# Kernel optimization log

Measured on AMD Instinct MI355X. Metric: run time of the kernel, lower is better.

Reference implementation:

```python
import jax, jax.numpy as jnp
import numpy as np

EPS = 1e-6

def rmsnorm(x, scale):
    return x * jax.lax.rsqrt(jnp.mean(x * x, axis=-1, keepdims=True) + EPS) * scale

def setup_inputs() -> dict:
    key = jax.random.key(0)
    ks = jax.random.split(key, 8)
    B1, B2 = 16, 64
    D, H, A = 8192, 1024, 2          # deter_size, hidden_size, action_size
    S, C, G = 32, 64, 8              # stoch_size, classes, blocks
    sc = 0.02                        # trunc-normal-ish init scale
    f32 = jnp.float32
    return dict(
        deter=jax.random.normal(ks[0], (B1, B2, D), f32),
        stoch=jax.random.normal(ks[1], (B1, B2, S, C), f32),
        action=jax.random.normal(ks[2], (B1, B2, A), f32),
        W1=(jax.random.normal(ks[3], (H, D), f32) * sc),
        b1=jnp.zeros((H,), f32),
        s1=jnp.ones((H,), f32),
        W2=(jax.random.normal(ks[4], (H, S * C), f32) * sc),
        b2=jnp.zeros((H,), f32),
        s2=jnp.ones((H,), f32),
        W3=(jax.random.normal(ks[5], (H, A), f32) * sc),
        b3=jnp.zeros((H,), f32),
        s3=jnp.ones((H,), f32),
        Wb1=(jax.random.normal(ks[6], (G, (3 * G * H + D) // G, D // G), f32) * sc),
        bb1=jnp.zeros((D,), f32),
        sb1=jnp.ones((D,), f32),
        Wb2=(jax.random.normal(ks[7], (G, D // G, 3 * D // G), f32) * sc),
        bb2=jnp.zeros((3 * D,), f32),
    )

def reference(deter, stoch, action, W1, b1, s1, W2, b2, s2, W3, b3, s3, Wb1, bb1, sb1, Wb2, bb2):
    batch_shape = deter.shape[:-1]
    D = deter.shape[-1]
    d = deter.reshape(-1, D)                       # (B, D)
    B = d.shape[0]
    G = Wb1.shape[0]
    H = W1.shape[0]
    s = stoch.reshape(B, -1)                       # (B, S*C)
    a = action.reshape(B, -1)                      # (B, A)
    a = a / jax.lax.stop_gradient(jnp.maximum(1.0, jnp.abs(a)))
    # three parallel Linear + RMSNorm + SiLU branches
    x1 = jax.nn.silu(rmsnorm(d @ W1.T + b1, s1))
    x2 = jax.nn.silu(rmsnorm(s @ W2.T + b2, s2))
    x3 = jax.nn.silu(rmsnorm(a @ W3.T + b3, s3))
    x = jnp.concatenate([x1, x2, x3], axis=-1)     # (B, 3H)
    x = jnp.broadcast_to(x[:, None, :], (B, G, 3 * H))
    x = jnp.concatenate([x, d.reshape(B, G, D // G)], axis=-1)  # (B, G, 3H + D/G)
    # block-diagonal grouped GEMM + RMSNorm + SiLU (dyn_layers=1)
    h = jnp.einsum('bgi,gio->bgo', x, Wb1).reshape(B, D) + bb1
    h = jax.nn.silu(rmsnorm(h, sb1))
    # final block-diagonal GEMM -> 3*D gate pre-activations
    y = jnp.einsum('bgi,gio->bgo', h.reshape(B, G, D // G), Wb2).reshape(B, 3 * D) + bb2
    r, c, u = jnp.split(y.reshape(B, G, -1), 3, axis=-1)        # each (B, G, D/G)
    reset = jax.nn.sigmoid(r.reshape(B, D))
    cand = jnp.tanh(reset * c.reshape(B, D))
    update = jax.nn.sigmoid(u.reshape(B, D) - 1.0)
    next_deter = update * cand + (1.0 - update) * d
    return next_deter.reshape(*batch_shape, D)
```

## Files before the change

### kernel.cpp

```cpp
#include <hip/hip_runtime.h>
#include <stdint.h>

typedef unsigned short ushort_t;
typedef __attribute__((ext_vector_type(8))) short bf16x8;
typedef __attribute__((ext_vector_type(4))) float f32x4;

#define EPS 1e-6f

__device__ __forceinline__ float b2f(ushort_t u) {
    union { uint32_t i; float f; } v; v.i = ((uint32_t)u) << 16; return v.f;
}
__device__ __forceinline__ ushort_t f2b(float f) {
    union { float f; uint32_t i; } v; v.f = f;
    uint32_t x = v.i;
    uint32_t r = (x + 0x7fffu + ((x >> 16) & 1u)) >> 16;
    return (ushort_t)r;
}

__device__ __forceinline__ void async_copy16(const void* g, void* l) {
    __builtin_amdgcn_global_load_lds(
        (const __attribute__((address_space(1))) uint32_t*)(uintptr_t)g,
        (__attribute__((address_space(3))) uint32_t*)(uintptr_t)l,
        16, 0, 0);
}

__global__ __launch_bounds__(256) void cast4_k(
    const float* __restrict__ s0, ushort_t* __restrict__ d0, int n0,
    const float* __restrict__ s1, ushort_t* __restrict__ d1, int n1,
    const float* __restrict__ s2, ushort_t* __restrict__ d2, int n2,
    const float* __restrict__ s3, ushort_t* __restrict__ d3) {
    int j = blockIdx.x * 256 + threadIdx.x;
    const float* s; ushort_t* d;
    if (j < n0) { s = s0; d = d0; }
    else if ((j -= n0) < n1) { s = s1; d = d1; }
    else if ((j -= n1) < n2) { s = s2; d = d2; }
    else { j -= n2; s = s3; d = d3; }
    float4 v = ((const float4*)s)[j];
    ushort4 o;
    o.x = f2b(v.x); o.y = f2b(v.y); o.z = f2b(v.z); o.w = f2b(v.w);
    ((ushort4*)d)[j] = o;
}

__global__ __launch_bounds__(256) void transpose_cast_k(const float* __restrict__ src,
                                                        ushort_t* __restrict__ dst,
                                                        int R, int C) {
    __shared__ float tile[32][33];
    int bat = blockIdx.z;
    int c0 = blockIdx.x * 32, r0 = blockIdx.y * 32;
    const float* s = src + (size_t)bat * R * C;
    ushort_t* d = dst + (size_t)bat * R * C;
    int tx = threadIdx.x, ty = threadIdx.y;
    float4 v = *(const float4*)&s[(size_t)(r0 + ty) * C + c0 + tx * 4];
    tile[ty][tx * 4 + 0] = v.x;
    tile[ty][tx * 4 + 1] = v.y;
    tile[ty][tx * 4 + 2] = v.z;
    tile[ty][tx * 4 + 3] = v.w;
    __syncthreads();
    ushort4 o;
    o.x = f2b(tile[tx * 4 + 0][ty]);
    o.y = f2b(tile[tx * 4 + 1][ty]);
    o.z = f2b(tile[tx * 4 + 2][ty]);
    o.w = f2b(tile[tx * 4 + 3][ty]);
    *(ushort4*)&d[(size_t)(c0 + ty) * R + r0 + tx * 4] = o;
}

template <int MODE, bool OUT_BF16, int BM, int BN, int WNW>
__global__ __launch_bounds__(WNW * 128, 2) void gemm_bt_k(
    const ushort_t* __restrict__ Aa, const ushort_t* __restrict__ Ab,
    const ushort_t* __restrict__ Bw,
    float* __restrict__ Cf, ushort_t* __restrict__ Cb,
    int lda, int ldb, int ldc, int Ksl, int k0base, int czoff) {
    constexpr int THREADS = WNW * 128;
    constexpr int MR = (BM / 2) / 16;
    constexpr int NR = (BN / WNW) / 16;
    constexpr int SR = THREADS >> 3;
    __shared__ __align__(16) ushort_t As[2][BM * 64];
    __shared__ __align__(16) ushort_t Bs[2][BN * 64];
    const int tid = threadIdx.x;

    const int gx = gridDim.x;
    const int nxy = gx * gridDim.y;
    const int flat = blockIdx.x + blockIdx.y * gx;
    const int cpx = nxy >> 3;
    const int L = (flat & 7) * cpx + (flat >> 3);
    const int bm = L % gx, bn = L / gx;
    const int bz = blockIdx.z;
    const int k0 = k0base + bz * Ksl;
    const int m0 = bm * BM, n0 = bn * BN;
    const int cz = bz * czoff;
    const int lane = tid & 63, w = tid >> 6;
    const int wm = (w & 1) * (BM / 2);
    const int wn = (w >> 1) * (BN / WNW);

    f32x4 acc[MR][NR];
#pragma unroll
    for (int i = 0; i < MR; i++)
#pragma unroll
        for (int j = 0; j < NR; j++) acc[i][j] = (f32x4){0.f, 0.f, 0.f, 0.f};

    auto a_ptr = [&](int m, int kk) -> const ushort_t* {
        if (MODE == 0) {
            return Aa + (size_t)m * lda + kk;
        } else if (MODE == 1) {
            if (kk < 3072) return Aa + (size_t)m * 3072 + kk;
            int g = n0 >> 10;
            return Ab + (size_t)m * 8192 + g * 1024 + (kk - 3072);
        } else {
            int g = n0 / 3072;
            return Aa + (size_t)m * 8192 + g * 1024 + kk;
        }
    };

    const int srow = tid >> 3;
    const int sslot = tid & 7;
    const int gco = (sslot ^ (srow & 7)) << 3;
    const int lco = sslot << 3;

    auto stage = [&](int buf, int kk) {
#pragma unroll
        for (int p = 0; p < BM / SR; ++p) {
            int r = p * SR + srow;
            async_copy16(a_ptr(m0 + r, kk + gco), &As[buf][r * 64 + lco]);
        }
#pragma unroll
        for (int p = 0; p < BN / SR; ++p) {
            int r = p * SR + srow;
            async_copy16(Bw + (size_t)(n0 + r) * ldb + kk + gco, &Bs[buf][r * 64 + lco]);
        }
    };

    const int nt = Ksl >> 6;
    stage(0, k0);
    __builtin_amdgcn_sched_barrier(0);

    const int qc = lane >> 4;
    const int rl = lane & 15;
    int cur = 0;

    for (int t = 0; t < nt; ++t) {
        if (t + 1 < nt) {
            stage(cur ^ 1, k0 + ((t + 1) << 6));
            asm volatile("s_waitcnt vmcnt(8)" ::: "memory");
        } else {
            asm volatile("s_waitcnt vmcnt(0)" ::: "memory");
        }
        __builtin_amdgcn_s_barrier();
        __builtin_amdgcn_sched_barrier(0);

#pragma unroll
        for (int h = 0; h < 2; ++h) {
            bf16x8 af[MR], bfr[NR];
#pragma unroll
            for (int i = 0; i < MR; i++) {
                int ra = wm + i * 16 + rl;
                int slot = ((h << 2) + qc) ^ (ra & 7);
                af[i] = *(const bf16x8*)&As[cur][ra * 64 + (slot << 3)];
            }
#pragma unroll
            for (int j = 0; j < NR; j++) {
                int rb = wn + j * 16 + rl;
                int slot = ((h << 2) + qc) ^ (rb & 7);
                bfr[j] = *(const bf16x8*)&Bs[cur][rb * 64 + (slot << 3)];
            }
#pragma unroll
            for (int i = 0; i < MR; i++)
#pragma unroll
                for (int j = 0; j < NR; j++)
                    acc[i][j] = __builtin_amdgcn_mfma_f32_16x16x32_bf16(af[i], bfr[j], acc[i][j], 0, 0, 0);
        }

        if (t + 1 < nt) {
            __builtin_amdgcn_sched_barrier(0);
            __builtin_amdgcn_s_barrier();
            __builtin_amdgcn_sched_barrier(0);
            cur ^= 1;
        }
    }

    const int cr = (lane >> 4) * 4, cc = lane & 15;
#pragma unroll
    for (int i = 0; i < MR; i++) {
#pragma unroll
        for (int j = 0; j < NR; j++) {
#pragma unroll
            for (int r = 0; r < 4; r++) {
                int row = m0 + wm + i * 16 + cr + r;
                int col = n0 + cz + wn + j * 16 + cc;
                float v = acc[i][j][r];
                if (OUT_BF16) {
                    Cb[(size_t)row * ldc + col] = f2b(v);
                } else {
                    Cf[(size_t)row * ldc + col] = v;
                }
            }
        }
    }
}

__global__ __launch_bounds__(256) void branch3_k(const float* __restrict__ act,
                                                 const float* __restrict__ W3,
                                                 float* __restrict__ xacc) {
    int idx = blockIdx.x * 256 + threadIdx.x;
    int b = idx >> 10, h = idx & 1023;
    float a0 = act[b * 2 + 0], a1 = act[b * 2 + 1];
    a0 = a0 / fmaxf(1.f, fabsf(a0));
    a1 = a1 / fmaxf(1.f, fabsf(a1));
    float v = a0 * W3[h * 2 + 0] + a1 * W3[h * 2 + 1];
    xacc[(size_t)b * 7168 + 6144 + h] = v;
}

__global__ __launch_bounds__(256) void norm_silu_1024_k(
    const float* __restrict__ xacc,
    const float* __restrict__ b1, const float* __restrict__ s1,
    const float* __restrict__ b2, const float* __restrict__ s2,
    const float* __restrict__ b3, const float* __restrict__ s3,
    ushort_t* __restrict__ xbf) {
    int b = blockIdx.x, c = blockIdx.y, tid = threadIdx.x;
    const float* bias = (c == 0) ? b1 : (c == 1) ? b2 : b3;
    const float* scl  = (c == 0) ? s1 : (c == 1) ? s2 : s3;
    const float* row = xacc + (size_t)b * 7168 + ((c == 0) ? 0 : (c == 1) ? 4096 : 6144);
    const int np = (c == 0) ? 4 : (c == 1) ? 2 : 1;
    float4 v = ((const float4*)row)[tid];
#pragma unroll 4
    for (int p = 1; p < np; ++p) {
        float4 t = ((const float4*)(row + p * 1024))[tid];
        v.x += t.x; v.y += t.y; v.z += t.z; v.w += t.w;
    }
    float4 bb = ((const float4*)bias)[tid];
    v.x += bb.x; v.y += bb.y; v.z += bb.z; v.w += bb.w;
    float ss = v.x * v.x + v.y * v.y + v.z * v.z + v.w * v.w;
#pragma unroll
    for (int off = 32; off > 0; off >>= 1) ss += __shfl_down(ss, off, 64);
    __shared__ float wsum[4];
    int lane = tid & 63, wid = tid >> 6;
    if (lane == 0) wsum[wid] = ss;
    __syncthreads();
    float tot = wsum[0] + wsum[1] + wsum[2] + wsum[3];
    float rms = rsqrtf(tot * (1.0f / 1024.0f) + EPS);
    float4 sc = ((const float4*)scl)[tid];
    float o0 = v.x * rms * sc.x; o0 = o0 / (1.f + __expf(-o0));
    float o1 = v.y * rms * sc.y; o1 = o1 / (1.f + __expf(-o1));
    float o2 = v.z * rms * sc.z; o2 = o2 / (1.f + __expf(-o2));
    float o3 = v.w * rms * sc.w; o3 = o3 / (1.f + __expf(-o3));
    ushort4 o; o.x = f2b(o0); o.y = f2b(o1); o.z = f2b(o2); o.w = f2b(o3);
    ((ushort4*)(xbf + (size_t)b * 3072 + c * 1024))[tid] = o;
}

__global__ __launch_bounds__(256) void norm_silu_8192_k(const float* __restrict__ hpre,
                                                        const float* __restrict__ bb1,
                                                        const float* __restrict__ sb1,
                                                        ushort_t* __restrict__ hbf) {
    int b = blockIdx.x, tid = threadIdx.x;
    const float4* src = (const float4*)(hpre + (size_t)b * 16384);
    float4 v[8];
    float ss = 0.f;
#pragma unroll
    for (int k = 0; k < 8; k++) {
        float4 t = src[tid + k * 256];
        float4 u = src[tid + k * 256 + 2048];
        t.x += u.x; t.y += u.y; t.z += u.z; t.w += u.w;
        float4 bv = ((const float4*)bb1)[tid + k * 256];
        t.x += bv.x; t.y += bv.y; t.z += bv.z; t.w += bv.w;
        v[k] = t;
        ss += t.x * t.x + t.y * t.y + t.z * t.z + t.w * t.w;
    }
#pragma unroll
    for (int off = 32; off > 0; off >>= 1) ss += __shfl_down(ss, off, 64);
    __shared__ float wsum[4];
    int lane = tid & 63, wid = tid >> 6;
    if (lane == 0) wsum[wid] = ss;
    __syncthreads();
    float tot = wsum[0] + wsum[1] + wsum[2] + wsum[3];
    float rms = rsqrtf(tot * (1.0f / 8192.0f) + EPS);
    ushort_t* dst = hbf + (size_t)b * 8192;
#pragma unroll
    for (int k = 0; k < 8; k++) {
        float4 sv = ((const float4*)sb1)[tid + k * 256];
        float o0 = v[k].x * rms * sv.x; o0 = o0 / (1.f + __expf(-o0));
        float o1 = v[k].y * rms * sv.y; o1 = o1 / (1.f + __expf(-o1));
        float o2 = v[k].z * rms * sv.z; o2 = o2 / (1.f + __expf(-o2));
        float o3 = v[k].w * rms * sv.w; o3 = o3 / (1.f + __expf(-o3));
        ushort4 o; o.x = f2b(o0); o.y = f2b(o1); o.z = f2b(o2); o.w = f2b(o3);
        ((ushort4*)dst)[tid + k * 256] = o;
    }
}

__global__ __launch_bounds__(256) void gates_k(const ushort_t* __restrict__ y,
                                               const float* __restrict__ bb2,
                                               const float* __restrict__ deter,
                                               float* __restrict__ out) {
    int idx = blockIdx.x * 256 + threadIdx.x;
    int f = idx * 4;
    int b = f >> 13, d = f & 8191;
    int g = d >> 10, j = d & 1023;
    size_t ybase = (size_t)b * 24576 + g * 3072 + j;
    ushort4 rv = *(const ushort4*)(y + ybase);
    ushort4 cv = *(const ushort4*)(y + ybase + 1024);
    ushort4 uv = *(const ushort4*)(y + ybase + 2048);
    float4 bbr = *(const float4*)(bb2 + g * 3072 + j);
    float4 bbc = *(const float4*)(bb2 + g * 3072 + 1024 + j);
    float4 bbu = *(const float4*)(bb2 + g * 3072 + 2048 + j);
    float4 dv = *(const float4*)(deter + f);
    float rr[4] = {b2f(rv.x) + bbr.x, b2f(rv.y) + bbr.y, b2f(rv.z) + bbr.z, b2f(rv.w) + bbr.w};
    float cc[4] = {b2f(cv.x) + bbc.x, b2f(cv.y) + bbc.y, b2f(cv.z) + bbc.z, b2f(cv.w) + bbc.w};
    float uu[4] = {b2f(uv.x) + bbu.x, b2f(uv.y) + bbu.y, b2f(uv.z) + bbu.z, b2f(uv.w) + bbu.w};
    float dd[4] = {dv.x, dv.y, dv.z, dv.w};
    float oo[4];
#pragma unroll
    for (int t = 0; t < 4; t++) {
        float reset = 1.f / (1.f + __expf(-rr[t]));
        float cand = tanhf(reset * cc[t]);
        float upd = 1.f / (1.f + __expf(-(uu[t] - 1.f)));
        oo[t] = upd * cand + (1.f - upd) * dd[t];
    }
    float4 o; o.x = oo[0]; o.y = oo[1]; o.z = oo[2]; o.w = oo[3];
    *(float4*)(out + f) = o;
}

extern "C" void kernel_launch(void* const* d_in, const int* in_sizes, int n_in,
                              void* d_out, int out_size, void* d_ws, size_t ws_size,
                              hipStream_t stream) {
    const float* deter = (const float*)d_in[0];
    const float* stoch = (const float*)d_in[1];
    const float* action = (const float*)d_in[2];
    const float* W1 = (const float*)d_in[3];
    const float* b1 = (const float*)d_in[4];
    const float* s1 = (const float*)d_in[5];
    const float* W2 = (const float*)d_in[6];
    const float* b2 = (const float*)d_in[7];
    const float* s2 = (const float*)d_in[8];
    const float* W3 = (const float*)d_in[9];
    const float* b3 = (const float*)d_in[10];
    const float* s3 = (const float*)d_in[11];
    const float* Wb1 = (const float*)d_in[12];
    const float* bb1 = (const float*)d_in[13];
    const float* sb1 = (const float*)d_in[14];
    const float* Wb2 = (const float*)d_in[15];
    const float* bb2 = (const float*)d_in[16];
    float* out = (float*)d_out;

    char* ws = (char*)d_ws;
    ushort_t* dbf   = (ushort_t*)(ws + 0);
    ushort_t* sbf   = (ushort_t*)(ws + 16777216);
    ushort_t* W1bf  = (ushort_t*)(ws + 20971520);
    ushort_t* W2bf  = (ushort_t*)(ws + 37748736);
    ushort_t* Wb1T  = (ushort_t*)(ws + 41943040);
    ushort_t* Wb2T  = (ushort_t*)(ws + 109051904);
    ushort_t* xbf   = (ushort_t*)(ws + 159383552);
    float*    hpre2 = (float*)   (ws + 165675008);
    ushort_t* hbf   = (ushort_t*)(ws + 232783872);
    float*    xacc = hpre2;
    ushort_t* ybf  = (ushort_t*)hpre2;

    cast4_k<<<20480, 256, 0, stream>>>(deter, dbf, 2097152,
                                       stoch, sbf, 524288,
                                       W1, W1bf, 2097152,
                                       W2, W2bf);
    transpose_cast_k<<<dim3(32, 128, 8), dim3(8, 32), 0, stream>>>(Wb1, Wb1T, 4096, 1024);
    transpose_cast_k<<<dim3(96, 32, 8), dim3(8, 32), 0, stream>>>(Wb2, Wb2T, 1024, 3072);

    gemm_bt_k<0, false, 128, 128, 2><<<dim3(8, 8, 4), 256, 0, stream>>>(
        dbf, nullptr, W1bf, xacc, nullptr, 8192, 8192, 7168, 2048, 0, 1024);
    gemm_bt_k<0, false, 128, 128, 2><<<dim3(8, 8, 2), 256, 0, stream>>>(
        sbf, nullptr, W2bf, xacc + 4096, nullptr, 2048, 2048, 7168, 1024, 0, 1024);
    branch3_k<<<4096, 256, 0, stream>>>(action, W3, xacc);

    norm_silu_1024_k<<<dim3(1024, 3), 256, 0, stream>>>(xacc, b1, s1, b2, s2, b3, s3, xbf);

    gemm_bt_k<1, false, 256, 256, 4><<<dim3(4, 32, 2), 512, 0, stream>>>(
        xbf, dbf, Wb1T, hpre2, nullptr, 0, 4096, 16384, 2048, 0, 8192);

    norm_silu_8192_k<<<1024, 256, 0, stream>>>(hpre2, bb1, sb1, hbf);

    gemm_bt_k<2, true, 256, 256, 4><<<dim3(4, 96, 1), 512, 0, stream>>>(
        hbf, nullptr, Wb2T, nullptr, ybf, 0, 1024, 24576, 1024, 0, 0);

    gates_k<<<8192, 256, 0, stream>>>(ybf, bb2, deter, out);
}
```

Measured before the change: 586.8 us.

## Add multi-stage LDS pipeline with smaller K tile for large block GEMMs

Parameterizes the GEMM kernel by K-tile size and pipeline depth, and switches the two large 256x256 block-diagonal GEMMs to a 4-buffer, 3-deep prefetch with BK=32. More tiles are kept in flight to hide global-load latency, and the LDS footprint stays about the same. The cost is more iterations and more barriers per K step, and the XOR swizzle is narrower, which may raise LDS bank conflicts. The smaller GEMMs keep their previous configuration.

Result: slower. 604.6 us (+3.0%).

```diff
diff --git a/kernel.cpp b/kernel.cpp
--- a/kernel.cpp
+++ b/kernel.cpp
@@ -22,6 +22,16 @@
         (const __attribute__((address_space(1))) uint32_t*)(uintptr_t)g,
         (__attribute__((address_space(3))) uint32_t*)(uintptr_t)l,
         16, 0, 0);
+}
+
+template <int N>
+__device__ __forceinline__ void wait_vmcnt() {
+    if constexpr (N == 0)       asm volatile("s_waitcnt vmcnt(0)" ::: "memory");
+    else if constexpr (N == 4)  asm volatile("s_waitcnt vmcnt(4)" ::: "memory");
+    else if constexpr (N == 8)  asm volatile("s_waitcnt vmcnt(8)" ::: "memory");
+    else if constexpr (N == 12) asm volatile("s_waitcnt vmcnt(12)" ::: "memory");
+    else if constexpr (N == 16) asm volatile("s_waitcnt vmcnt(16)" ::: "memory");
+    else if constexpr (N == 24) asm volatile("s_waitcnt vmcnt(24)" ::: "memory");
 }
 
 __global__ __launch_bounds__(256) void cast4_k(
@@ -64,7 +74,7 @@
     *(ushort4*)&d[(size_t)(c0 + ty) * R + r0 + tx * 4] = o;
 }
 
-template <int MODE, bool OUT_BF16, int BM, int BN, int WNW>
+template <int MODE, bool OUT_BF16, int BM, int BN, int WNW, int BK, int DEPTH>
 __global__ __launch_bounds__(WNW * 128, 2) void gemm_bt_k(
     const ushort_t* __restrict__ Aa, const ushort_t* __restrict__ Ab,
     const ushort_t* __restrict__ Bw,
@@ -73,9 +83,13 @@
     constexpr int THREADS = WNW * 128;
     constexpr int MR = (BM / 2) / 16;
     constexpr int NR = (BN / WNW) / 16;
-    constexpr int SR = THREADS >> 3;
-    __shared__ __align__(16) ushort_t As[2][BM * 64];
-    __shared__ __align__(16) ushort_t Bs[2][BN * 64];
+    constexpr int CS = BK / 8;
+    constexpr int SR = THREADS / CS;
+    constexpr int LPT = (BM + BN) / SR;
+    constexpr int NBUF = DEPTH + 1;
+    constexpr int HALVES = BK / 32;
+    __shared__ __align__(16) ushort_t As[NBUF][BM * BK];
+    __shared__ __align__(16) ushort_t Bs[NBUF][BN * BK];
     const int tid = threadIdx.x;
 
     const int gx = gridDim.x;
@@ -111,56 +125,70 @@
         }
     };
 
-    const int srow = tid >> 3;
-    const int sslot = tid & 7;
-    const int gco = (sslot ^ (srow & 7)) << 3;
+    const int srow = tid / CS;
+    const int sslot = tid % CS;
+    const int gco = (sslot ^ (srow & (CS - 1))) << 3;
     const int lco = sslot << 3;
 
     auto stage = [&](int buf, int kk) {
 #pragma unroll
         for (int p = 0; p < BM / SR; ++p) {
             int r = p * SR + srow;
-            async_copy16(a_ptr(m0 + r, kk + gco), &As[buf][r * 64 + lco]);
+            async_copy16(a_ptr(m0 + r, kk + gco), &As[buf][r * BK + lco]);
         }
 #pragma unroll
         for (int p = 0; p < BN / SR; ++p) {
             int r = p * SR + srow;
-            async_copy16(Bw + (size_t)(n0 + r) * ldb + kk + gco, &Bs[buf][r * 64 + lco]);
+            async_copy16(Bw + (size_t)(n0 + r) * ldb + kk + gco, &Bs[buf][r * BK + lco]);
         }
     };
 
-    const int nt = Ksl >> 6;
-    stage(0, k0);
+    const int nt = Ksl / BK;
+#pragma unroll
+    for (int d = 0; d < DEPTH; ++d) stage(d, k0 + d * BK);
     __builtin_amdgcn_sched_barrier(0);
 
     const int qc = lane >> 4;
     const int rl = lane & 15;
-    int cur = 0;
 
     for (int t = 0; t < nt; ++t) {
-        if (t + 1 < nt) {
-            stage(cur ^ 1, k0 + ((t + 1) << 6));
-            asm volatile("s_waitcnt vmcnt(8)" ::: "memory");
+        const int cur = t & (NBUF - 1);
+        if constexpr (DEPTH == 1) {
+            if (t + 1 < nt) {
+                stage((t + 1) & 1, k0 + (t + 1) * BK);
+                wait_vmcnt<LPT>();
+            } else {
+                wait_vmcnt<0>();
+            }
         } else {
-            asm volatile("s_waitcnt vmcnt(0)" ::: "memory");
+            if (t + 3 < nt) {
+                stage((t + 3) & 3, k0 + (t + 3) * BK);
+                wait_vmcnt<3 * LPT>();
+            } else if (t + 2 < nt) {
+                wait_vmcnt<2 * LPT>();
+            } else if (t + 1 < nt) {
+                wait_vmcnt<LPT>();
+            } else {
+                wait_vmcnt<0>();
+            }
         }
         __builtin_amdgcn_s_barrier();
         __builtin_amdgcn_sched_barrier(0);
 
 #pragma unroll
-        for (int h = 0; h < 2; ++h) {
+        for (int h = 0; h < HALVES; ++h) {
             bf16x8 af[MR], bfr[NR];
 #pragma unroll
             for (int i = 0; i < MR; i++) {
                 int ra = wm + i * 16 + rl;
-                int slot = ((h << 2) + qc) ^ (ra & 7);
-                af[i] = *(const bf16x8*)&As[cur][ra * 64 + (slot << 3)];
+                int slot = ((h << 2) + qc) ^ (ra & (CS - 1));
+                af[i] = *(const bf16x8*)&As[cur][ra * BK + (slot << 3)];
             }
 #pragma unroll
             for (int j = 0; j < NR; j++) {
                 int rb = wn + j * 16 + rl;
-                int slot = ((h << 2) + qc) ^ (rb & 7);
-                bfr[j] = *(const bf16x8*)&Bs[cur][rb * 64 + (slot << 3)];
+                int slot = ((h << 2) + qc) ^ (rb & (CS - 1));
+                bfr[j] = *(const bf16x8*)&Bs[cur][rb * BK + (slot << 3)];
             }
 #pragma unroll
             for (int i = 0; i < MR; i++)
@@ -173,7 +201,6 @@
             __builtin_amdgcn_sched_barrier(0);
             __builtin_amdgcn_s_barrier();
             __builtin_amdgcn_sched_barrier(0);
-            cur ^= 1;
         }
     }
 
@@ -359,20 +386,20 @@
     transpose_cast_k<<<dim3(32, 128, 8), dim3(8, 32), 0, stream>>>(Wb1, Wb1T, 4096, 1024);
     transpose_cast_k<<<dim3(96, 32, 8), dim3(8, 32), 0, stream>>>(Wb2, Wb2T, 1024, 3072);
 
-    gemm_bt_k<0, false, 128, 128, 2><<<dim3(8, 8, 4), 256, 0, stream>>>(
+    gemm_bt_k<0, false, 128, 128, 2, 64, 1><<<dim3(8, 8, 4), 256, 0, stream>>>(
         dbf, nullptr, W1bf, xacc, nullptr, 8192, 8192, 7168, 2048, 0, 1024);
-    gemm_bt_k<0, false, 128, 128, 2><<<dim3(8, 8, 2), 256, 0, stream>>>(
+    gemm_bt_k<0, false, 128, 128, 2, 64, 1><<<dim3(8, 8, 2), 256, 0, stream>>>(
         sbf, nullptr, W2bf, xacc + 4096, nullptr, 2048, 2048, 7168, 1024, 0, 1024);
     branch3_k<<<4096, 256, 0, stream>>>(action, W3, xacc);
 
     norm_silu_1024_k<<<dim3(1024, 3), 256, 0, stream>>>(xacc, b1, s1, b2, s2, b3, s3, xbf);
 
-    gemm_bt_k<1, false, 256, 256, 4><<<dim3(4, 32, 2), 512, 0, stream>>>(
+    gemm_bt_k<1, false, 256, 256, 4, 32, 3><<<dim3(4, 32, 2), 512, 0, stream>>>(
         xbf, dbf, Wb1T, hpre2, nullptr, 0, 4096, 16384, 2048, 0, 8192);
 
     norm_silu_8192_k<<<1024, 256, 0, stream>>>(hpre2, bb1, sb1, hbf);
 
-    gemm_bt_k<2, true, 256, 256, 4><<<dim3(4, 96, 1), 512, 0, stream>>>(
+    gemm_bt_k<2, true, 256, 256, 4, 32, 3><<<dim3(4, 96, 1), 512, 0, stream>>>(
         hbf, nullptr, Wb2T, nullptr, ybf, 0, 1024, 24576, 1024, 0, 0);
 
     gates_k<<<8192, 256, 0, stream>>>(ybf, bb2, deter, out);
```
